# Kernel optimization log

Hardware: AMD Instinct MI355X
Metric: run time of the kernel (lower is better)

The kernel has to match this reference:

```python
import jax, jax.numpy as jnp
import numpy as np

ADIM = 128
VDIM = 64

def setup_inputs() -> dict:
    key = jax.random.key(0)
    ks = jax.random.split(key, 12)
    B, N, E = 4, 10000, 320000
    pos_0 = jax.random.normal(ks[0], (B, N, 3), dtype=jnp.float32)
    pos_1 = jax.random.normal(ks[1], (B, N, 3), dtype=jnp.float32)
    src = jax.random.randint(ks[2], (E,), 0, N, dtype=jnp.int64)
    dst = jax.random.randint(ks[3], (E,), 0, N, dtype=jnp.int64)
    # parameters (torch default inits approximated; randn for VecLinear as in source)
    Wv = jax.random.normal(ks[4], (VDIM, 6), dtype=jnp.float32)
    def lin(k, fan_in, fan_out):
        kw, kb = jax.random.split(k)
        bound = 1.0 / np.sqrt(fan_in)
        W = jax.random.uniform(kw, (fan_out, fan_in), minval=-bound, maxval=bound, dtype=jnp.float32)
        b = jax.random.uniform(kb, (fan_out,), minval=-bound, maxval=bound, dtype=jnp.float32)
        return W, b
    W1, b1 = lin(ks[5], 6, ADIM)
    W2, b2 = lin(ks[6], ADIM, ADIM)
    W3, b3 = lin(ks[7], ADIM, ADIM)
    return {"pos_0": pos_0, "pos_1": pos_1, "src": src, "dst": dst,
            "Wv": Wv, "W1": W1, "b1": b1, "W2": W2, "b2": b2, "W3": W3, "b3": b3}

def _leaky(x):
    return jnp.where(x >= 0, x, 0.2 * x)

def reference(pos_0, pos_1, src, dst, Wv, W1, b1, W2, b2, W3, b3):
    # gather endpoint positions: (B, E, 3)
    p0s = jnp.take(pos_0, src, axis=1)
    p0d = jnp.take(pos_0, dst, axis=1)
    p1s = jnp.take(pos_1, src, axis=1)
    p1d = jnp.take(pos_1, dst, axis=1)
    # 6 relative vectors: (B, E, 6, 3)
    vecs = jnp.stack([p0d - p0s, p1d - p1s, p1s - p0s, p1d - p0d, p1s - p0d, p1d - p0s], axis=2)
    norms = jnp.sqrt(jnp.sum(vecs * vecs, axis=-1))  # (B, E, 6)
    h = _leaky(jnp.einsum('bei,oi->beo', norms, W1) + b1)
    h = _leaky(jnp.einsum('bei,oi->beo', h, W2) + b2)
    a_out = jnp.einsum('bei,oi->beo', h, W3) + b3  # (B, E, ADIM)
    v_out = jnp.einsum('oi,beik->beok', Wv, vecs) / 3  # (B, E, VDIM, 3)
    return (a_out, v_out)
```

## Files before the change

kernel.cpp:

```cpp
#include <hip/hip_runtime.h>

#define NB 4
#define NN 10000
#define NE 320000
#define EPB 64
#define NBLK ((NB * NE) / EPB)

typedef unsigned int uint;
typedef unsigned short ushort;
typedef __attribute__((ext_vector_type(8))) short short8;
typedef __attribute__((ext_vector_type(4))) float f32x4;

#define WS_W2F 0
#define WS_W3F 32768
#define WS_W1F 65536
#define WS_WV  73728

static __device__ __forceinline__ ushort f2bf(float f) {
    uint u = __float_as_uint(f);
    u += 0x7fffu + ((u >> 16) & 1u);
    return (ushort)(u >> 16);
}
static __device__ __forceinline__ uint pack2(float a, float b) {
    return (uint)f2bf(a) | ((uint)f2bf(b) << 16);
}
static __device__ __forceinline__ short8 u4s8(uint4 v) {
    union { uint4 u; short8 s; } x; x.u = v; return x.s;
}
static __device__ __forceinline__ float lk(float x) { return x >= 0.f ? x : 0.2f * x; }

__global__ void prep_kernel(const float* __restrict__ W1, const float* __restrict__ W2,
                            const float* __restrict__ W3, const float* __restrict__ Wv,
                            unsigned char* __restrict__ ws) {
    int tid = blockIdx.x * blockDim.x + threadIdx.x;
    if (tid < 4096) {
        const float* W = (tid < 2048) ? W2 : W3;
        uint4* dst = (uint4*)(ws + ((tid < 2048) ? WS_W2F : WS_W3F));
        int f = tid & 2047;
        int lane = f & 63, kt = (f >> 6) & 3, ct = (f >> 8) & 3, wn = (f >> 10) & 1;
        int a = lane >> 4, lm = lane & 15;
        int col = wn * 64 + ct * 16 + lm;
        uint w[4];
        #pragma unroll
        for (int jw = 0; jw < 4; ++jw) {
            int j0 = jw * 2, j1 = j0 + 1;
            int k0 = kt * 32 + (j0 >> 2) * 16 + a * 4 + (j0 & 3);
            int k1 = kt * 32 + (j1 >> 2) * 16 + a * 4 + (j1 & 3);
            w[jw] = pack2(W[col * 128 + k0], W[col * 128 + k1]);
        }
        dst[f] = make_uint4(w[0], w[1], w[2], w[3]);
    } else if (tid < 4608) {
        int f = tid - 4096;
        int lane = f & 63, ct = (f >> 6) & 3, wn = (f >> 8) & 1;
        int a = lane >> 4, lm = lane & 15;
        int col = wn * 64 + ct * 16 + lm;
        uint w[4];
        #pragma unroll
        for (int jw = 0; jw < 4; ++jw) {
            int j0 = jw * 2, j1 = j0 + 1;
            int k0 = (j0 >> 2) * 16 + a * 4 + (j0 & 3);
            int k1 = (j1 >> 2) * 16 + a * 4 + (j1 & 3);
            float f0 = (k0 < 6) ? W1[col * 6 + k0] : 0.f;
            float f1 = (k1 < 6) ? W1[col * 6 + k1] : 0.f;
            w[jw] = pack2(f0, f1);
        }
        ((uint4*)(ws + WS_W1F))[f] = make_uint4(w[0], w[1], w[2], w[3]);
    } else if (tid < 5120) {
        int s = tid - 4608;
        int o = s >> 3, i = s & 7;
        ((float*)(ws + WS_WV))[s] = (i < 6) ? Wv[o * 6 + i] * (1.f / 3.f) : 0.f;
    }
}

__global__ __launch_bounds__(256, 2)
void edge_kernel(const float* __restrict__ pos0, const float* __restrict__ pos1,
                 const int* __restrict__ src, const int* __restrict__ dstI,
                 const float* __restrict__ b1, const float* __restrict__ b2,
                 const float* __restrict__ b3,
                 const unsigned char* __restrict__ ws, float* __restrict__ out) {
    __shared__ float s_pts[64][13];
    __shared__ float s_vecs[64][28];
    __shared__ uint4 s_H1[256];
    __shared__ float s_hf[64 * 128];

    const int tid = threadIdx.x;
    const int lane = tid & 63;
    const int wid = tid >> 6;
    const int wm = wid >> 1;
    const int wn = wid & 1;
    const int lm = lane & 15;
    const int la = lane >> 4;

    const int bid = blockIdx.x;
    const int b = bid / (NE / EPB);
    const int e0 = (bid % (NE / EPB)) * EPB;

    const uint4* W1F = (const uint4*)(ws + WS_W1F);
    const uint4* W2F = (const uint4*)(ws + WS_W2F);
    const uint4* W3F = (const uint4*)(ws + WS_W3F);
    uint4 w1f[4], w2f[4][4], w3f[4][4];
    #pragma unroll
    for (int ct = 0; ct < 4; ++ct) w1f[ct] = W1F[(wn * 4 + ct) * 64 + lane];
    #pragma unroll
    for (int ct = 0; ct < 4; ++ct)
        #pragma unroll
        for (int kt = 0; kt < 4; ++kt) {
            int idx = ((wn * 4 + ct) * 4 + kt) * 64 + lane;
            w2f[ct][kt] = W2F[idx];
            w3f[ct][kt] = W3F[idx];
        }
    float b1c[4], b2c[4], b3c[4];
    #pragma unroll
    for (int ct = 0; ct < 4; ++ct) {
        int col = wn * 64 + ct * 16 + lm;
        b1c[ct] = b1[col];
        b2c[ct] = b2[col];
        b3c[ct] = b3[col];
    }

    {
        int le = tid & 63;
        int pt = tid >> 6;
        int e = e0 + le;
        int node = (pt & 1) ? dstI[e] : src[e];
        const float* P = (pt < 2) ? pos0 : pos1;
        const float* p = P + ((size_t)b * NN + node) * 3;
        s_pts[le][pt * 3 + 0] = p[0];
        s_pts[le][pt * 3 + 1] = p[1];
        s_pts[le][pt * 3 + 2] = p[2];
    }
    __syncthreads();

    {
        const int row = tid & 63;
        const int w = tid >> 6;
        uint4 hf = make_uint4(0, 0, 0, 0);
        if (w == 0) {
            float P[12];
            #pragma unroll
            for (int i = 0; i < 12; ++i) P[i] = s_pts[row][i];
            const int va[4] = {1, 3, 2, 3}, vb[4] = {0, 2, 0, 1};
            float v[4][3], n[4];
            #pragma unroll
            for (int i = 0; i < 4; ++i) {
                #pragma unroll
                for (int c = 0; c < 3; ++c) v[i][c] = P[va[i] * 3 + c] - P[vb[i] * 3 + c];
                n[i] = sqrtf(v[i][0] * v[i][0] + v[i][1] * v[i][1] + v[i][2] * v[i][2]);
            }
            float4 t0 = {v[0][0], v[0][1], v[0][2], v[1][0]};
            float4 t1 = {v[1][1], v[1][2], v[2][0], v[2][1]};
            float4 t2 = {v[2][2], v[3][0], v[3][1], v[3][2]};
            *(float4*)&s_vecs[row][0] = t0;
            *(float4*)&s_vecs[row][4] = t1;
            *(float4*)&s_vecs[row][8] = t2;
            hf.x = pack2(n[0], n[1]);
            hf.y = pack2(n[2], n[3]);
        } else if (w == 1) {
            float P[12];
            #pragma unroll
            for (int i = 0; i < 12; ++i) P[i] = s_pts[row][i];
            float v4[3], v5[3];
            #pragma unroll
            for (int c = 0; c < 3; ++c) {
                v4[c] = P[6 + c] - P[3 + c];
                v5[c] = P[9 + c] - P[0 + c];
            }
            float n4 = sqrtf(v4[0] * v4[0] + v4[1] * v4[1] + v4[2] * v4[2]);
            float n5 = sqrtf(v5[0] * v5[0] + v5[1] * v5[1] + v5[2] * v5[2]);
            float4 t = {v4[0], v4[1], v4[2], v5[0]};
            *(float4*)&s_vecs[row][12] = t;
            float2 t2 = {v5[1], v5[2]};
            *(float2*)&s_vecs[row][16] = t2;
            hf.x = pack2(n4, n5);
        }
        s_H1[(row >> 4) * 64 + w * 16 + (row & 15)] = hf;
    }
    __syncthreads();

    const f32x4 zero4 = {0.f, 0.f, 0.f, 0.f};
    short8 afh[2];
    afh[0] = u4s8(s_H1[(wm * 2 + 0) * 64 + lane]);
    afh[1] = u4s8(s_H1[(wm * 2 + 1) * 64 + lane]);
    f32x4 acc1[2][4];
    #pragma unroll
    for (int mtl = 0; mtl < 2; ++mtl)
        #pragma unroll
        for (int ct = 0; ct < 4; ++ct) {
            acc1[mtl][ct] = __builtin_amdgcn_mfma_f32_16x16x32_bf16(
                afh[mtl], u4s8(w1f[ct]), zero4, 0, 0, 0);
        }
    #pragma unroll
    for (int mtl = 0; mtl < 2; ++mtl)
        #pragma unroll
        for (int ct = 0; ct < 4; ++ct) {
            const int col = wn * 64 + ct * 16 + lm;
            #pragma unroll
            for (int r = 0; r < 4; ++r) {
                int row = wm * 32 + mtl * 16 + la * 4 + r;
                s_hf[row * 128 + (col ^ ((row & 7) << 2))] = lk(acc1[mtl][ct][r] + b1c[ct]);
            }
        }
    __syncthreads();

    const int swR = (lm & 7) << 2;
    uint4 af2[2][4];
    #pragma unroll
    for (int mtl = 0; mtl < 2; ++mtl) {
        const int row = wm * 32 + mtl * 16 + lm;
        const float* hrow = &s_hf[row * 128];
        #pragma unroll
        for (int kt = 0; kt < 4; ++kt) {
            float4 lo = *(const float4*)&hrow[(kt * 32 + la * 4) ^ swR];
            float4 hi = *(const float4*)&hrow[(kt * 32 + 16 + la * 4) ^ swR];
            af2[mtl][kt] = make_uint4(pack2(lo.x, lo.y), pack2(lo.z, lo.w),
                                      pack2(hi.x, hi.y), pack2(hi.z, hi.w));
        }
    }
    __syncthreads();

    f32x4 acc2[2][4];
    #pragma unroll
    for (int mtl = 0; mtl < 2; ++mtl)
        #pragma unroll
        for (int ct = 0; ct < 4; ++ct) acc2[mtl][ct] = zero4;
    #pragma unroll
    for (int kt = 0; kt < 4; ++kt)
        #pragma unroll
        for (int ct = 0; ct < 4; ++ct)
            #pragma unroll
            for (int mtl = 0; mtl < 2; ++mtl)
                acc2[mtl][ct] = __builtin_amdgcn_mfma_f32_16x16x32_bf16(
                    u4s8(af2[mtl][kt]), u4s8(w2f[ct][kt]), acc2[mtl][ct], 0, 0, 0);
    #pragma unroll
    for (int mtl = 0; mtl < 2; ++mtl)
        #pragma unroll
        for (int ct = 0; ct < 4; ++ct) {
            const int col = wn * 64 + ct * 16 + lm;
            #pragma unroll
            for (int r = 0; r < 4; ++r) {
                int row = wm * 32 + mtl * 16 + la * 4 + r;
                s_hf[row * 128 + (col ^ ((row & 7) << 2))] = lk(acc2[mtl][ct][r] + b2c[ct]);
            }
        }
    __syncthreads();

    uint4 af3[2][4];
    #pragma unroll
    for (int mtl = 0; mtl < 2; ++mtl) {
        const int row = wm * 32 + mtl * 16 + lm;
        const float* hrow = &s_hf[row * 128];
        #pragma unroll
        for (int kt = 0; kt < 4; ++kt) {
            float4 lo = *(const float4*)&hrow[(kt * 32 + la * 4) ^ swR];
            float4 hi = *(const float4*)&hrow[(kt * 32 + 16 + la * 4) ^ swR];
            af3[mtl][kt] = make_uint4(pack2(lo.x, lo.y), pack2(lo.z, lo.w),
                                      pack2(hi.x, hi.y), pack2(hi.z, hi.w));
        }
    }
    __syncthreads();

    f32x4 acc3[2][4];
    #pragma unroll
    for (int mtl = 0; mtl < 2; ++mtl)
        #pragma unroll
        for (int ct = 0; ct < 4; ++ct) acc3[mtl][ct] = zero4;
    #pragma unroll
    for (int kt = 0; kt < 4; ++kt)
        #pragma unroll
        for (int ct = 0; ct < 4; ++ct)
            #pragma unroll
            for (int mtl = 0; mtl < 2; ++mtl)
                acc3[mtl][ct] = __builtin_amdgcn_mfma_f32_16x16x32_bf16(
                    u4s8(af3[mtl][kt]), u4s8(w3f[ct][kt]), acc3[mtl][ct], 0, 0, 0);
    #pragma unroll
    for (int mtl = 0; mtl < 2; ++mtl)
        #pragma unroll
        for (int ct = 0; ct < 4; ++ct) {
            const int col = wn * 64 + ct * 16 + lm;
            #pragma unroll
            for (int r = 0; r < 4; ++r) {
                int row = wm * 32 + mtl * 16 + la * 4 + r;
                s_hf[row * 128 + (col ^ ((row & 7) << 2))] = acc3[mtl][ct][r] + b3c[ct];
            }
        }
    __syncthreads();

    const size_t aBase = ((size_t)b * NE + e0) * 128;
    #pragma unroll
    for (int i = 0; i < 8; ++i) {
        int f = i * 256 + tid;
        int row = f >> 5;
        int c4 = (f & 31) << 2;
        float4 v = *(const float4*)&s_hf[row * 128 + (c4 ^ ((row & 7) << 2))];
        *(float4*)&out[aBase + (size_t)f * 4] = v;
    }
    __syncthreads();

    const int seg = tid & 7;
    const int eL = tid >> 3;
    float4 wvr[16];
    const float4* WVp = (const float4*)(ws + WS_WV);
    #pragma unroll
    for (int j = 0; j < 16; ++j) wvr[j] = WVp[seg * 16 + j];
    float* s_V = s_hf;
    const size_t vBase = (size_t)NB * NE * 128 + ((size_t)b * NE + e0) * 192;
    #pragma unroll
    for (int h = 0; h < 2; ++h) {
        const int e = h * 32 + eL;
        float vv[18];
        {
            float4 a0 = *(const float4*)&s_vecs[e][0];
            float4 a1 = *(const float4*)&s_vecs[e][4];
            float4 a2 = *(const float4*)&s_vecs[e][8];
            float4 a3 = *(const float4*)&s_vecs[e][12];
            vv[0] = a0.x; vv[1] = a0.y; vv[2] = a0.z; vv[3] = a0.w;
            vv[4] = a1.x; vv[5] = a1.y; vv[6] = a1.z; vv[7] = a1.w;
            vv[8] = a2.x; vv[9] = a2.y; vv[10] = a2.z; vv[11] = a2.w;
            vv[12] = a3.x; vv[13] = a3.y; vv[14] = a3.z; vv[15] = a3.w;
            vv[16] = s_vecs[e][16]; vv[17] = s_vecs[e][17];
        }
        float buf[24];
        #pragma unroll
        for (int oo = 0; oo < 8; ++oo) {
            float4 wlo = wvr[oo * 2], whi = wvr[oo * 2 + 1];
            #pragma unroll
            for (int k = 0; k < 3; ++k) {
                float r = wlo.x * vv[k];
                r = fmaf(wlo.y, vv[3 + k], r);
                r = fmaf(wlo.z, vv[6 + k], r);
                r = fmaf(wlo.w, vv[9 + k], r);
                r = fmaf(whi.x, vv[12 + k], r);
                r = fmaf(whi.y, vv[15 + k], r);
                buf[oo * 3 + k] = r;
            }
        }
        #pragma unroll
        for (int w4 = 0; w4 < 6; ++w4) {
            float4 t = {buf[w4 * 4], buf[w4 * 4 + 1], buf[w4 * 4 + 2], buf[w4 * 4 + 3]};
            *(float4*)&s_V[eL * 196 + seg * 24 + w4 * 4] = t;
        }
        __syncthreads();
        #pragma unroll
        for (int i = 0; i < 6; ++i) {
            int f4 = i * 256 + tid;
            int ef = f4 / 48;
            int r4 = (f4 - ef * 48) * 4;
            float4 v = *(const float4*)&s_V[ef * 196 + r4];
            *(float4*)&out[vBase + (size_t)h * 6144 + (size_t)f4 * 4] = v;
        }
        __syncthreads();
    }
}

extern "C" void kernel_launch(void* const* d_in, const int* in_sizes, int n_in,
                              void* d_out, int out_size, void* d_ws, size_t ws_size,
                              hipStream_t stream) {
    const float* pos0 = (const float*)d_in[0];
    const float* pos1 = (const float*)d_in[1];
    const int* src = (const int*)d_in[2];
    const int* dstI = (const int*)d_in[3];
    const float* Wv = (const float*)d_in[4];
    const float* W1 = (const float*)d_in[5];
    const float* b1 = (const float*)d_in[6];
    const float* W2 = (const float*)d_in[7];
    const float* b2 = (const float*)d_in[8];
    const float* W3 = (const float*)d_in[9];
    const float* b3 = (const float*)d_in[10];
    unsigned char* ws = (unsigned char*)d_ws;
    float* out = (float*)d_out;

    prep_kernel<<<dim3(20), dim3(256), 0, stream>>>(W1, W2, W3, Wv, ws);
    edge_kernel<<<dim3(NBLK), dim3(256), 0, stream>>>(pos0, pos1, src, dstI, b1, b2, b3, ws, out);
}
```

Baseline: 472.7 us.

## Transpose MLP to weight-as-A MFMA and compute vector output on MFMA

```diff
diff --git a/kernel.cpp b/kernel.cpp
--- a/kernel.cpp
+++ b/kernel.cpp
@@ -11,10 +11,10 @@
 typedef __attribute__((ext_vector_type(8))) short short8;
 typedef __attribute__((ext_vector_type(4))) float f32x4;
 
-#define WS_W2F 0
-#define WS_W3F 32768
-#define WS_W1F 65536
-#define WS_WV  73728
+#define WS_W1T 0
+#define WS_W2T 8192
+#define WS_W3T 40960
+#define WS_WVT 73728
 
 static __device__ __forceinline__ ushort f2bf(float f) {
     uint u = __float_as_uint(f);
@@ -35,88 +35,87 @@
     int tid = blockIdx.x * blockDim.x + threadIdx.x;
     if (tid < 4096) {
         const float* W = (tid < 2048) ? W2 : W3;
-        uint4* dst = (uint4*)(ws + ((tid < 2048) ? WS_W2F : WS_W3F));
+        uint4* dst = (uint4*)(ws + ((tid < 2048) ? WS_W2T : WS_W3T));
         int f = tid & 2047;
-        int lane = f & 63, kt = (f >> 6) & 3, ct = (f >> 8) & 3, wn = (f >> 10) & 1;
-        int a = lane >> 4, lm = lane & 15;
-        int col = wn * 64 + ct * 16 + lm;
+        int lane = f & 63, kt = (f >> 6) & 3, mt = (f >> 8) & 7;
+        int la = lane >> 4, lm = lane & 15;
+        int n = mt * 16 + lm;
         uint w[4];
         #pragma unroll
         for (int jw = 0; jw < 4; ++jw) {
             int j0 = jw * 2, j1 = j0 + 1;
-            int k0 = kt * 32 + (j0 >> 2) * 16 + a * 4 + (j0 & 3);
-            int k1 = kt * 32 + (j1 >> 2) * 16 + a * 4 + (j1 & 3);
-            w[jw] = pack2(W[col * 128 + k0], W[col * 128 + k1]);
+            int k0 = kt * 32 + (j0 >> 2) * 16 + la * 4 + (j0 & 3);
+            int k1 = kt * 32 + (j1 >> 2) * 16 + la * 4 + (j1 & 3);
+            w[jw] = pack2(W[n * 128 + k0], W[n * 128 + k1]);
         }
         dst[f] = make_uint4(w[0], w[1], w[2], w[3]);
     } else if (tid < 4608) {
         int f = tid - 4096;
-        int lane = f & 63, ct = (f >> 6) & 3, wn = (f >> 8) & 1;
-        int a = lane >> 4, lm = lane & 15;
-        int col = wn * 64 + ct * 16 + lm;
+        int lane = f & 63, mt = f >> 6;
+        int la = lane >> 4, lm = lane & 15;
+        int n = mt * 16 + lm;
         uint w[4];
         #pragma unroll
         for (int jw = 0; jw < 4; ++jw) {
             int j0 = jw * 2, j1 = j0 + 1;
-            int k0 = (j0 >> 2) * 16 + a * 4 + (j0 & 3);
-            int k1 = (j1 >> 2) * 16 + a * 4 + (j1 & 3);
-            float f0 = (k0 < 6) ? W1[col * 6 + k0] : 0.f;
-            float f1 = (k1 < 6) ? W1[col * 6 + k1] : 0.f;
+            int k0 = (j0 >> 2) * 16 + la * 4 + (j0 & 3);
+            int k1 = (j1 >> 2) * 16 + la * 4 + (j1 & 3);
+            float f0 = (k0 < 6) ? W1[n * 6 + k0] : 0.f;
+            float f1 = (k1 < 6) ? W1[n * 6 + k1] : 0.f;
             w[jw] = pack2(f0, f1);
         }
-        ((uint4*)(ws + WS_W1F))[f] = make_uint4(w[0], w[1], w[2], w[3]);
-    } else if (tid < 5120) {
-        int s = tid - 4608;
-        int o = s >> 3, i = s & 7;
-        ((float*)(ws + WS_WV))[s] = (i < 6) ? Wv[o * 6 + i] * (1.f / 3.f) : 0.f;
-    }
-}
-
-__global__ __launch_bounds__(256, 2)
+        ((uint4*)(ws + WS_W1T))[f] = make_uint4(w[0], w[1], w[2], w[3]);
+    } else if (tid < 5376) {
+        int f = tid - 4608;
+        int lane = f & 63, mt = f >> 6;
+        int la = lane >> 4, lm = lane & 15;
+        int row = mt * 16 + lm;
+        int o = row / 3, c = row - o * 3;
+        uint w[4];
+        #pragma unroll
+        for (int jw = 0; jw < 4; ++jw) {
+            float vv[2];
+            #pragma unroll
+            for (int dc = 0; dc < 2; ++dc) {
+                int j = jw * 2 + dc;
+                int k = (j >> 2) * 16 + la * 4 + (j & 3);
+                int i = k / 3, cc = k - i * 3;
+                vv[dc] = (k < 18 && cc == c) ? Wv[o * 6 + i] * (1.f / 3.f) : 0.f;
+            }
+            w[jw] = pack2(vv[0], vv[1]);
+        }
+        ((uint4*)(ws + WS_WVT))[f] = make_uint4(w[0], w[1], w[2], w[3]);
+    }
+}
+
+__global__ __launch_bounds__(256, 3)
 void edge_kernel(const float* __restrict__ pos0, const float* __restrict__ pos1,
                  const int* __restrict__ src, const int* __restrict__ dstI,
                  const float* __restrict__ b1, const float* __restrict__ b2,
                  const float* __restrict__ b3,
                  const unsigned char* __restrict__ ws, float* __restrict__ out) {
     __shared__ float s_pts[64][13];
-    __shared__ float s_vecs[64][28];
-    __shared__ uint4 s_H1[256];
-    __shared__ float s_hf[64 * 128];
+    __shared__ float s_vecs[64][20];
+    __shared__ float s_norms[8][64];
+    __shared__ uint4 s_B[16 * 64];
 
     const int tid = threadIdx.x;
     const int lane = tid & 63;
     const int wid = tid >> 6;
-    const int wm = wid >> 1;
-    const int wn = wid & 1;
+    const int wm = wid & 1;
+    const int wn = wid >> 1;
     const int lm = lane & 15;
     const int la = lane >> 4;
 
     const int bid = blockIdx.x;
     const int b = bid / (NE / EPB);
     const int e0 = (bid % (NE / EPB)) * EPB;
-
-    const uint4* W1F = (const uint4*)(ws + WS_W1F);
-    const uint4* W2F = (const uint4*)(ws + WS_W2F);
-    const uint4* W3F = (const uint4*)(ws + WS_W3F);
-    uint4 w1f[4], w2f[4][4], w3f[4][4];
-    #pragma unroll
-    for (int ct = 0; ct < 4; ++ct) w1f[ct] = W1F[(wn * 4 + ct) * 64 + lane];
-    #pragma unroll
-    for (int ct = 0; ct < 4; ++ct)
-        #pragma unroll
-        for (int kt = 0; kt < 4; ++kt) {
-            int idx = ((wn * 4 + ct) * 4 + kt) * 64 + lane;
-            w2f[ct][kt] = W2F[idx];
-            w3f[ct][kt] = W3F[idx];
-        }
-    float b1c[4], b2c[4], b3c[4];
-    #pragma unroll
-    for (int ct = 0; ct < 4; ++ct) {
-        int col = wn * 64 + ct * 16 + lm;
-        b1c[ct] = b1[col];
-        b2c[ct] = b2[col];
-        b3c[ct] = b3[col];
-    }
+    const size_t eg0 = (size_t)b * NE + e0;
+
+    const uint4* W1T = (const uint4*)(ws + WS_W1T);
+    const uint4* W2T = (const uint4*)(ws + WS_W2T);
+    const uint4* W3T = (const uint4*)(ws + WS_W3T);
+    const uint4* WVT = (const uint4*)(ws + WS_WVT);
 
     {
         int le = tid & 63;
@@ -134,18 +133,17 @@
     {
         const int row = tid & 63;
         const int w = tid >> 6;
-        uint4 hf = make_uint4(0, 0, 0, 0);
         if (w == 0) {
             float P[12];
             #pragma unroll
             for (int i = 0; i < 12; ++i) P[i] = s_pts[row][i];
-            const int va[4] = {1, 3, 2, 3}, vb[4] = {0, 2, 0, 1};
-            float v[4][3], n[4];
+            const int va[4] = {1, 3, 2, 3}, vb_[4] = {0, 2, 0, 1};
+            float v[4][3];
             #pragma unroll
             for (int i = 0; i < 4; ++i) {
                 #pragma unroll
-                for (int c = 0; c < 3; ++c) v[i][c] = P[va[i] * 3 + c] - P[vb[i] * 3 + c];
-                n[i] = sqrtf(v[i][0] * v[i][0] + v[i][1] * v[i][1] + v[i][2] * v[i][2]);
+                for (int c = 0; c < 3; ++c) v[i][c] = P[va[i] * 3 + c] - P[vb_[i] * 3 + c];
+                s_norms[i][row] = sqrtf(v[i][0]*v[i][0] + v[i][1]*v[i][1] + v[i][2]*v[i][2]);
             }
             float4 t0 = {v[0][0], v[0][1], v[0][2], v[1][0]};
             float4 t1 = {v[1][1], v[1][2], v[2][0], v[2][1]};
@@ -153,8 +151,6 @@
             *(float4*)&s_vecs[row][0] = t0;
             *(float4*)&s_vecs[row][4] = t1;
             *(float4*)&s_vecs[row][8] = t2;
-            hf.x = pack2(n[0], n[1]);
-            hf.y = pack2(n[2], n[3]);
         } else if (w == 1) {
             float P[12];
             #pragma unroll
@@ -165,190 +161,177 @@
                 v4[c] = P[6 + c] - P[3 + c];
                 v5[c] = P[9 + c] - P[0 + c];
             }
-            float n4 = sqrtf(v4[0] * v4[0] + v4[1] * v4[1] + v4[2] * v4[2]);
-            float n5 = sqrtf(v5[0] * v5[0] + v5[1] * v5[1] + v5[2] * v5[2]);
+            s_norms[4][row] = sqrtf(v4[0]*v4[0] + v4[1]*v4[1] + v4[2]*v4[2]);
+            s_norms[5][row] = sqrtf(v5[0]*v5[0] + v5[1]*v5[1] + v5[2]*v5[2]);
             float4 t = {v4[0], v4[1], v4[2], v5[0]};
             *(float4*)&s_vecs[row][12] = t;
             float2 t2 = {v5[1], v5[2]};
             *(float2*)&s_vecs[row][16] = t2;
-            hf.x = pack2(n4, n5);
-        }
-        s_H1[(row >> 4) * 64 + w * 16 + (row & 15)] = hf;
+        }
     }
     __syncthreads();
 
     const f32x4 zero4 = {0.f, 0.f, 0.f, 0.f};
-    short8 afh[2];
-    afh[0] = u4s8(s_H1[(wm * 2 + 0) * 64 + lane]);
-    afh[1] = u4s8(s_H1[(wm * 2 + 1) * 64 + lane]);
-    f32x4 acc1[2][4];
-    #pragma unroll
-    for (int mtl = 0; mtl < 2; ++mtl)
-        #pragma unroll
-        for (int ct = 0; ct < 4; ++ct) {
-            acc1[mtl][ct] = __builtin_amdgcn_mfma_f32_16x16x32_bf16(
-                afh[mtl], u4s8(w1f[ct]), zero4, 0, 0, 0);
-        }
-    #pragma unroll
-    for (int mtl = 0; mtl < 2; ++mtl)
-        #pragma unroll
-        for (int ct = 0; ct < 4; ++ct) {
-            const int col = wn * 64 + ct * 16 + lm;
-            #pragma unroll
-            for (int r = 0; r < 4; ++r) {
-                int row = wm * 32 + mtl * 16 + la * 4 + r;
-                s_hf[row * 128 + (col ^ ((row & 7) << 2))] = lk(acc1[mtl][ct][r] + b1c[ct]);
-            }
-        }
-    __syncthreads();
-
-    const int swR = (lm & 7) << 2;
-    uint4 af2[2][4];
-    #pragma unroll
-    for (int mtl = 0; mtl < 2; ++mtl) {
-        const int row = wm * 32 + mtl * 16 + lm;
-        const float* hrow = &s_hf[row * 128];
-        #pragma unroll
-        for (int kt = 0; kt < 4; ++kt) {
-            float4 lo = *(const float4*)&hrow[(kt * 32 + la * 4) ^ swR];
-            float4 hi = *(const float4*)&hrow[(kt * 32 + 16 + la * 4) ^ swR];
-            af2[mtl][kt] = make_uint4(pack2(lo.x, lo.y), pack2(lo.z, lo.w),
-                                      pack2(hi.x, hi.y), pack2(hi.z, hi.w));
-        }
-    }
-    __syncthreads();
-
-    f32x4 acc2[2][4];
-    #pragma unroll
-    for (int mtl = 0; mtl < 2; ++mtl)
-        #pragma unroll
-        for (int ct = 0; ct < 4; ++ct) acc2[mtl][ct] = zero4;
-    #pragma unroll
-    for (int kt = 0; kt < 4; ++kt)
-        #pragma unroll
-        for (int ct = 0; ct < 4; ++ct)
-            #pragma unroll
-            for (int mtl = 0; mtl < 2; ++mtl)
-                acc2[mtl][ct] = __builtin_amdgcn_mfma_f32_16x16x32_bf16(
-                    u4s8(af2[mtl][kt]), u4s8(w2f[ct][kt]), acc2[mtl][ct], 0, 0, 0);
-    #pragma unroll
-    for (int mtl = 0; mtl < 2; ++mtl)
-        #pragma unroll
-        for (int ct = 0; ct < 4; ++ct) {
-            const int col = wn * 64 + ct * 16 + lm;
-            #pragma unroll
-            for (int r = 0; r < 4; ++r) {
-                int row = wm * 32 + mtl * 16 + la * 4 + r;
-                s_hf[row * 128 + (col ^ ((row & 7) << 2))] = lk(acc2[mtl][ct][r] + b2c[ct]);
-            }
-        }
-    __syncthreads();
-
-    uint4 af3[2][4];
-    #pragma unroll
-    for (int mtl = 0; mtl < 2; ++mtl) {
-        const int row = wm * 32 + mtl * 16 + lm;
-        const float* hrow = &s_hf[row * 128];
-        #pragma unroll
-        for (int kt = 0; kt < 4; ++kt) {
-            float4 lo = *(const float4*)&hrow[(kt * 32 + la * 4) ^ swR];
-            float4 hi = *(const float4*)&hrow[(kt * 32 + 16 + la * 4) ^ swR];
-            af3[mtl][kt] = make_uint4(pack2(lo.x, lo.y), pack2(lo.z, lo.w),
-                                      pack2(hi.x, hi.y), pack2(hi.z, hi.w));
-        }
-    }
-    __syncthreads();
-
-    f32x4 acc3[2][4];
-    #pragma unroll
-    for (int mtl = 0; mtl < 2; ++mtl)
-        #pragma unroll
-        for (int ct = 0; ct < 4; ++ct) acc3[mtl][ct] = zero4;
-    #pragma unroll
-    for (int kt = 0; kt < 4; ++kt)
-        #pragma unroll
-        for (int ct = 0; ct < 4; ++ct)
-            #pragma unroll
-            for (int mtl = 0; mtl < 2; ++mtl)
-                acc3[mtl][ct] = __builtin_amdgcn_mfma_f32_16x16x32_bf16(
-                    u4s8(af3[mtl][kt]), u4s8(w3f[ct][kt]), acc3[mtl][ct], 0, 0, 0);
-    #pragma unroll
-    for (int mtl = 0; mtl < 2; ++mtl)
-        #pragma unroll
-        for (int ct = 0; ct < 4; ++ct) {
-            const int col = wn * 64 + ct * 16 + lm;
-            #pragma unroll
-            for (int r = 0; r < 4; ++r) {
-                int row = wm * 32 + mtl * 16 + la * 4 + r;
-                s_hf[row * 128 + (col ^ ((row & 7) << 2))] = acc3[mtl][ct][r] + b3c[ct];
-            }
-        }
-    __syncthreads();
-
-    const size_t aBase = ((size_t)b * NE + e0) * 128;
-    #pragma unroll
-    for (int i = 0; i < 8; ++i) {
-        int f = i * 256 + tid;
-        int row = f >> 5;
-        int c4 = (f & 31) << 2;
-        float4 v = *(const float4*)&s_hf[row * 128 + (c4 ^ ((row & 7) << 2))];
-        *(float4*)&out[aBase + (size_t)f * 4] = v;
-    }
-    __syncthreads();
-
-    const int seg = tid & 7;
-    const int eL = tid >> 3;
-    float4 wvr[16];
-    const float4* WVp = (const float4*)(ws + WS_WV);
-    #pragma unroll
-    for (int j = 0; j < 16; ++j) wvr[j] = WVp[seg * 16 + j];
-    float* s_V = s_hf;
-    const size_t vBase = (size_t)NB * NE * 128 + ((size_t)b * NE + e0) * 192;
-    #pragma unroll
-    for (int h = 0; h < 2; ++h) {
-        const int e = h * 32 + eL;
-        float vv[18];
-        {
-            float4 a0 = *(const float4*)&s_vecs[e][0];
-            float4 a1 = *(const float4*)&s_vecs[e][4];
-            float4 a2 = *(const float4*)&s_vecs[e][8];
-            float4 a3 = *(const float4*)&s_vecs[e][12];
-            vv[0] = a0.x; vv[1] = a0.y; vv[2] = a0.z; vv[3] = a0.w;
-            vv[4] = a1.x; vv[5] = a1.y; vv[6] = a1.z; vv[7] = a1.w;
-            vv[8] = a2.x; vv[9] = a2.y; vv[10] = a2.z; vv[11] = a2.w;
-            vv[12] = a3.x; vv[13] = a3.y; vv[14] = a3.z; vv[15] = a3.w;
-            vv[16] = s_vecs[e][16]; vv[17] = s_vecs[e][17];
-        }
-        float buf[24];
-        #pragma unroll
-        for (int oo = 0; oo < 8; ++oo) {
-            float4 wlo = wvr[oo * 2], whi = wvr[oo * 2 + 1];
-            #pragma unroll
-            for (int k = 0; k < 3; ++k) {
-                float r = wlo.x * vv[k];
-                r = fmaf(wlo.y, vv[3 + k], r);
-                r = fmaf(wlo.z, vv[6 + k], r);
-                r = fmaf(wlo.w, vv[9 + k], r);
-                r = fmaf(whi.x, vv[12 + k], r);
-                r = fmaf(whi.y, vv[15 + k], r);
-                buf[oo * 3 + k] = r;
-            }
-        }
-        #pragma unroll
-        for (int w4 = 0; w4 < 6; ++w4) {
-            float4 t = {buf[w4 * 4], buf[w4 * 4 + 1], buf[w4 * 4 + 2], buf[w4 * 4 + 3]};
-            *(float4*)&s_V[eL * 196 + seg * 24 + w4 * 4] = t;
-        }
-        __syncthreads();
-        #pragma unroll
-        for (int i = 0; i < 6; ++i) {
-            int f4 = i * 256 + tid;
-            int ef = f4 / 48;
-            int r4 = (f4 - ef * 48) * 4;
-            float4 v = *(const float4*)&s_V[ef * 196 + r4];
-            *(float4*)&out[vBase + (size_t)h * 6144 + (size_t)f4 * 4] = v;
-        }
-        __syncthreads();
+    f32x4 acc[4][2];
+
+    {
+        uint4 vb1[2];
+        #pragma unroll
+        for (int nt = 0; nt < 2; ++nt) {
+            int e = (wn * 2 + nt) * 16 + lm;
+            uint c0 = 0, c1 = 0;
+            if (la == 0) {
+                c0 = pack2(s_norms[0][e], s_norms[1][e]);
+                c1 = pack2(s_norms[2][e], s_norms[3][e]);
+            } else if (la == 1) {
+                c0 = pack2(s_norms[4][e], s_norms[5][e]);
+            }
+            vb1[nt] = make_uint4(c0, c1, 0u, 0u);
+        }
+        uint4 w1f[4];
+        #pragma unroll
+        for (int mtl = 0; mtl < 4; ++mtl) w1f[mtl] = W1T[(wm * 4 + mtl) * 64 + lane];
+        #pragma unroll
+        for (int mtl = 0; mtl < 4; ++mtl)
+            #pragma unroll
+            for (int nt = 0; nt < 2; ++nt)
+                acc[mtl][nt] = __builtin_amdgcn_mfma_f32_16x16x32_bf16(
+                    u4s8(w1f[mtl]), u4s8(vb1[nt]), zero4, 0, 0, 0);
+    }
+    #pragma unroll
+    for (int mtl = 0; mtl < 4; ++mtl) {
+        float4 bc = *(const float4*)&b1[(wm * 4 + mtl) * 16 + la * 4];
+        #pragma unroll
+        for (int nt = 0; nt < 2; ++nt) {
+            acc[mtl][nt][0] = lk(acc[mtl][nt][0] + bc.x);
+            acc[mtl][nt][1] = lk(acc[mtl][nt][1] + bc.y);
+            acc[mtl][nt][2] = lk(acc[mtl][nt][2] + bc.z);
+            acc[mtl][nt][3] = lk(acc[mtl][nt][3] + bc.w);
+        }
+    }
+    #pragma unroll
+    for (int nt = 0; nt < 2; ++nt)
+        #pragma unroll
+        for (int t = 0; t < 2; ++t) {
+            f32x4 ha = acc[2 * t][nt], hb = acc[2 * t + 1][nt];
+            s_B[((wn * 2 + nt) * 4 + wm * 2 + t) * 64 + lane] =
+                make_uint4(pack2(ha[0], ha[1]), pack2(ha[2], ha[3]),
+                           pack2(hb[0], hb[1]), pack2(hb[2], hb[3]));
+        }
+    __syncthreads();
+
+    uint4 vb[2][4];
+    #pragma unroll
+    for (int nt = 0; nt < 2; ++nt)
+        #pragma unroll
+        for (int kt = 0; kt < 4; ++kt)
+            vb[nt][kt] = s_B[((wn * 2 + nt) * 4 + kt) * 64 + lane];
+    __syncthreads();
+
+    {
+        uint4 wf[4][4];
+        #pragma unroll
+        for (int mtl = 0; mtl < 4; ++mtl)
+            #pragma unroll
+            for (int kt = 0; kt < 4; ++kt)
+                wf[mtl][kt] = W2T[((wm * 4 + mtl) * 4 + kt) * 64 + lane];
+        #pragma unroll
+        for (int mtl = 0; mtl < 4; ++mtl)
+            #pragma unroll
+            for (int nt = 0; nt < 2; ++nt) acc[mtl][nt] = zero4;
+        #pragma unroll
+        for (int kt = 0; kt < 4; ++kt)
+            #pragma unroll
+            for (int mtl = 0; mtl < 4; ++mtl)
+                #pragma unroll
+                for (int nt = 0; nt < 2; ++nt)
+                    acc[mtl][nt] = __builtin_amdgcn_mfma_f32_16x16x32_bf16(
+                        u4s8(wf[mtl][kt]), u4s8(vb[nt][kt]), acc[mtl][nt], 0, 0, 0);
+    }
+    #pragma unroll
+    for (int mtl = 0; mtl < 4; ++mtl) {
+        float4 bc = *(const float4*)&b2[(wm * 4 + mtl) * 16 + la * 4];
+        #pragma unroll
+        for (int nt = 0; nt < 2; ++nt) {
+            acc[mtl][nt][0] = lk(acc[mtl][nt][0] + bc.x);
+            acc[mtl][nt][1] = lk(acc[mtl][nt][1] + bc.y);
+            acc[mtl][nt][2] = lk(acc[mtl][nt][2] + bc.z);
+            acc[mtl][nt][3] = lk(acc[mtl][nt][3] + bc.w);
+        }
+    }
+    #pragma unroll
+    for (int nt = 0; nt < 2; ++nt)
+        #pragma unroll
+        for (int t = 0; t < 2; ++t) {
+            f32x4 ha = acc[2 * t][nt], hb = acc[2 * t + 1][nt];
+            s_B[((wn * 2 + nt) * 4 + wm * 2 + t) * 64 + lane] =
+                make_uint4(pack2(ha[0], ha[1]), pack2(ha[2], ha[3]),
+                           pack2(hb[0], hb[1]), pack2(hb[2], hb[3]));
+        }
+    __syncthreads();
+
+    #pragma unroll
+    for (int nt = 0; nt < 2; ++nt)
+        #pragma unroll
+        for (int kt = 0; kt < 4; ++kt)
+            vb[nt][kt] = s_B[((wn * 2 + nt) * 4 + kt) * 64 + lane];
+
+    {
+        uint4 wf[4][4];
+        #pragma unroll
+        for (int mtl = 0; mtl < 4; ++mtl)
+            #pragma unroll
+            for (int kt = 0; kt < 4; ++kt)
+                wf[mtl][kt] = W3T[((wm * 4 + mtl) * 4 + kt) * 64 + lane];
+        #pragma unroll
+        for (int mtl = 0; mtl < 4; ++mtl)
+            #pragma unroll
+            for (int nt = 0; nt < 2; ++nt) acc[mtl][nt] = zero4;
+        #pragma unroll
+        for (int kt = 0; kt < 4; ++kt)
+            #pragma unroll
+            for (int mtl = 0; mtl < 4; ++mtl)
+                #pragma unroll
+                for (int nt = 0; nt < 2; ++nt)
+                    acc[mtl][nt] = __builtin_amdgcn_mfma_f32_16x16x32_bf16(
+                        u4s8(wf[mtl][kt]), u4s8(vb[nt][kt]), acc[mtl][nt], 0, 0, 0);
+    }
+    #pragma unroll
+    for (int mtl = 0; mtl < 4; ++mtl) {
+        float4 bc = *(const float4*)&b3[(wm * 4 + mtl) * 16 + la * 4];
+        #pragma unroll
+        for (int nt = 0; nt < 2; ++nt) {
+            float4 v = {acc[mtl][nt][0] + bc.x, acc[mtl][nt][1] + bc.y,
+                        acc[mtl][nt][2] + bc.z, acc[mtl][nt][3] + bc.w};
+            size_t e = eg0 + (wn * 2 + nt) * 16 + lm;
+            *(float4*)&out[e * 128 + (wm * 4 + mtl) * 16 + la * 4] = v;
+        }
+    }
+
+    {
+        uint4 vbv[2];
+        #pragma unroll
+        for (int nt = 0; nt < 2; ++nt) {
+            int e = (wn * 2 + nt) * 16 + lm;
+            int base = la * 4;
+            uint c0 = pack2(s_vecs[e][base], s_vecs[e][base + 1]);
+            uint c1 = pack2(s_vecs[e][base + 2], s_vecs[e][base + 3]);
+            uint c2 = (la == 0) ? pack2(s_vecs[e][16], s_vecs[e][17]) : 0u;
+            vbv[nt] = make_uint4(c0, c1, c2, 0u);
+        }
+        float* vout = out + (size_t)NB * NE * 128;
+        #pragma unroll
+        for (int m6 = 0; m6 < 6; ++m6) {
+            uint4 wv = WVT[(wm * 6 + m6) * 64 + lane];
+            #pragma unroll
+            for (int nt = 0; nt < 2; ++nt) {
+                f32x4 av = __builtin_amdgcn_mfma_f32_16x16x32_bf16(
+                    u4s8(wv), u4s8(vbv[nt]), zero4, 0, 0, 0);
+                size_t e = eg0 + (wn * 2 + nt) * 16 + lm;
+                float4 v = {av[0], av[1], av[2], av[3]};
+                *(float4*)&vout[e * 192 + (wm * 6 + m6) * 16 + la * 4] = v;
+            }
+        }
     }
 }
 
@@ -369,6 +352,6 @@
     unsigned char* ws = (unsigned char*)d_ws;
     float* out = (float*)d_out;
 
-    prep_kernel<<<dim3(20), dim3(256), 0, stream>>>(W1, W2, W3, Wv, ws);
+    prep_kernel<<<dim3(21), dim3(256), 0, stream>>>(W1, W2, W3, Wv, ws);
     edge_kernel<<<dim3(NBLK), dim3(256), 0, stream>>>(pos0, pos1, src, dstI, b1, b2, b3, ws, out);
 }
```

Measured after the change: 442.1 us. -6.5%, faster.
